# Kernel tuning notes

Measured on AMD Instinct MI355X. Metric: run time of the kernel, lower is better.

## Reference

```python
import jax, jax.numpy as jnp
import numpy as np


def setup_inputs() -> dict:
    key = jax.random.key(0)
    k1, k2, k3 = jax.random.split(key, 3)
    B, C, H, W = 32, 2048, 14, 14
    OUT = 512
    x = jax.random.normal(k1, (B, C, H, W), dtype=jnp.float32)
    gamma = jnp.zeros((1,), dtype=jnp.float32)  # nn.Parameter(torch.zeros(1))
    # 1x1 conv 2048 -> 512 (layer=4 branch), kaiming-ish scale
    conv_w = jax.random.normal(k2, (OUT, C, 1, 1), dtype=jnp.float32) * (1.0 / np.sqrt(C))
    conv_b = jax.random.normal(k3, (OUT,), dtype=jnp.float32) * 0.01
    return {"x": x, "gamma": gamma, "conv_w": conv_w, "conv_b": conv_b}


def reference(x, gamma, conv_w, conv_b):
    B, C, H, W = x.shape
    q = x.reshape(B, C, H * W)                      # [B, C, N]
    # energy[b, c, d] = <q[b,c,:], q[b,d,:]>
    energy = jnp.einsum('bcn,bdn->bcd', q, q)       # [B, C, C]
    # max-subtract trick: softmax(max - energy) along last dim
    energy_new = jnp.max(energy, axis=-1, keepdims=True) - energy
    attention = jax.nn.softmax(energy_new, axis=-1)  # [B, C, C]
    out = jnp.einsum('bcd,bdn->bcn', attention, q).reshape(B, C, H, W)
    out = gamma * out + x
    # 1x1 conv, stride 1, no padding (layer=4 branch)
    pam_out = jax.lax.conv_general_dilated(
        out, conv_w, window_strides=(1, 1), padding='VALID',
        dimension_numbers=('NCHW', 'OIHW', 'NCHW'))
    pam_out = pam_out + conv_b[None, :, None, None]
    return pam_out
```

## Files before the change

### kernel.cpp

```cpp
#include <hip/hip_runtime.h>
#include <hip/hip_bf16.h>
#include <stdint.h>

#define B_   32
#define C_   2048
#define HW_  196
#define OUT_ 512
#define KT_  128
#define NKT  (C_ / KT_)
#define BN_  64
#define PD_  4

typedef short short8 __attribute__((ext_vector_type(8)));
typedef float floatx4 __attribute__((ext_vector_type(4)));
typedef unsigned short u16;

#define VMCNT_WAIT(n) __builtin_amdgcn_s_waitcnt(0x0F70 | (n))

__device__ __forceinline__ uint32_t pack_bf16(float a, float b) {
  union { __hip_bfloat162 h; uint32_t u; } c;
  c.h = __float22bfloat162_rn(make_float2(a, b));
  return c.u;
}

__device__ __forceinline__ void async_ld16(const u16* g, void* lds_base) {
  __builtin_amdgcn_global_load_lds(
      (const __attribute__((address_space(1))) uint32_t*)g,
      (__attribute__((address_space(3))) uint32_t*)lds_base, 16, 0, 0);
}

__global__ void attn_fallback(const float* __restrict__ x, const float* __restrict__ gamma,
                              float* __restrict__ y) {
  float g = gamma[0];
  if (g == 0.0f) return;
  __shared__ float qc[HW_];
  __shared__ float e[C_];
  __shared__ float red[256];
  int tid = threadIdx.x;
  for (int cRow = blockIdx.x; cRow < C_; cRow += gridDim.x) {
    for (int b = 0; b < B_; ++b) {
      const float* q = x + (size_t)b * C_ * HW_;
      __syncthreads();
      for (int i = tid; i < HW_; i += 256) qc[i] = q[(size_t)cRow * HW_ + i];
      __syncthreads();
      for (int d = tid; d < C_; d += 256) {
        float s = 0.f;
        const float* qd = q + (size_t)d * HW_;
        for (int n = 0; n < HW_; ++n) s += qc[n] * qd[n];
        e[d] = s;
      }
      __syncthreads();
      float mn = 3.4e38f;
      for (int d = tid; d < C_; d += 256) mn = fminf(mn, e[d]);
      red[tid] = mn; __syncthreads();
      for (int s = 128; s > 0; s >>= 1) { if (tid < s) red[tid] = fminf(red[tid], red[tid + s]); __syncthreads(); }
      float emin = red[0];
      __syncthreads();
      float ps = 0.f;
      for (int d = tid; d < C_; d += 256) { float p = __expf(emin - e[d]); e[d] = p; ps += p; }
      red[tid] = ps; __syncthreads();
      for (int s = 128; s > 0; s >>= 1) { if (tid < s) red[tid] += red[tid + s]; __syncthreads(); }
      float S = red[0];
      __syncthreads();
      float invS = 1.f / S;
      for (int n = tid; n < HW_; n += 256) {
        float acc = 0.f;
        for (int d = 0; d < C_; ++d) acc += e[d] * q[(size_t)d * HW_ + n];
        y[((size_t)b * C_ + cRow) * HW_ + n] = g * acc * invS + q[(size_t)cRow * HW_ + n];
      }
    }
  }
}

__global__ __launch_bounds__(256, 3) void xposeW_kernel(
    const float* __restrict__ x, const float* __restrict__ ysrc,
    const float* __restrict__ gamma, u16* __restrict__ xT,
    const float* __restrict__ w, u16* __restrict__ wbf) {
  int tid = threadIdx.x;
  if (blockIdx.x >= 1024) {
    int gid = (blockIdx.x - 1024) * 256 + tid;
    float4 v = ((const float4*)w)[gid];
    ((uint2*)wbf)[gid] = make_uint2(pack_bf16(v.x, v.y), pack_bf16(v.z, v.w));
    return;
  }
  __shared__ float tile[64 * 197];
  const float* src = (gamma[0] != 0.f) ? ysrc : x;
  int b  = blockIdx.x >> 5;
  int c0 = (blockIdx.x & 31) * 64;
  const float* sb = src + ((size_t)b * C_ + c0) * HW_;
  for (int r = 0; r < 13; ++r) {
    int u = r * 256 + tid;
    if (u < 3136) {
      int ci = u / 49, n4 = u - ci * 49;
      float4 v = *(const float4*)(sb + (size_t)ci * HW_ + n4 * 4);
      float* tp = &tile[ci * 197 + n4 * 4];
      tp[0] = v.x; tp[1] = v.y; tp[2] = v.z; tp[3] = v.w;
    }
  }
  __syncthreads();
  u16* xTb = xT + (size_t)b * HW_ * C_ + c0;
  for (int r = 0; r < 7; ++r) {
    int u = r * 256 + tid;
    if (u < 1568) {
      int c8 = u & 7, n = u >> 3;
      const float* tp = &tile[c8 * 8 * 197 + n];
      uint4 o;
      o.x = pack_bf16(tp[0 * 197], tp[1 * 197]);
      o.y = pack_bf16(tp[2 * 197], tp[3 * 197]);
      o.z = pack_bf16(tp[4 * 197], tp[5 * 197]);
      o.w = pack_bf16(tp[6 * 197], tp[7 * 197]);
      *(uint4*)(xTb + (size_t)n * C_ + c8 * 8) = o;
    }
  }
}

__global__ __launch_bounds__(256, 2) void conv_gemm(
    const u16* __restrict__ xT, const u16* __restrict__ wbf,
    const float* __restrict__ bias, float* __restrict__ out) {

  __shared__ __align__(16) u16 Bs2[2][BN_ * KT_];

  int bid = blockIdx.x;
  int xcd = bid & 7;
  int s   = bid >> 3;
  int ot  = s & 3;
  int gl  = s >> 2;
  int grp = xcd * 16 + gl;
  int b   = grp >> 2;
  int nh  = grp & 3;
  int n0  = (nh < 3) ? nh * 64 : (HW_ - BN_);
  int oBase = ot * 128;

  int tid  = threadIdx.x;
  int wave = tid >> 6;
  int lane = tid & 63;
  int col  = lane & 15;
  int quad = lane >> 4;

  const u16* xTb  = xT + (size_t)b * HW_ * C_;
  const u16* aPtr = wbf + (size_t)(oBase + wave * 32 + col) * C_ + quad * 8;

  floatx4 acc[2][4];
#pragma unroll
  for (int m = 0; m < 2; ++m)
#pragma unroll
    for (int nt = 0; nt < 4; ++nt) { floatx4 z = {0.f, 0.f, 0.f, 0.f}; acc[m][nt] = z; }

  const u16* bPtr[PD_];
  int ldsOff[PD_];
#pragma unroll
  for (int jj = 0; jj < PD_; ++jj) {
    int rl = 4 * wave + quad + 16 * jj;
    int kc = col ^ (4 * wave + quad);
    bPtr[jj]   = xTb + (size_t)(n0 + rl) * C_ + kc * 8;
    ldsOff[jj] = (wave + 4 * jj) * 512;
  }

  uint4 aR[8];
  int aK = 0;
  auto loadA = [&]() {
#pragma unroll
    for (int m = 0; m < 2; ++m)
#pragma unroll
      for (int ks = 0; ks < 4; ++ks)
        aR[m * 4 + ks] = *(const uint4*)(aPtr + (size_t)m * 16 * C_ + aK + ks * 32);
    aK += KT_;
  };
  auto issueB = [&](u16* dst) {
#pragma unroll
    for (int jj = 0; jj < PD_; ++jj) {
      async_ld16(bPtr[jj], dst + ldsOff[jj]);
      bPtr[jj] += KT_;
    }
  };
  auto phase = [&](const u16* buf) {
    __builtin_amdgcn_s_setprio(1);
#pragma unroll
    for (int ks = 0; ks < 4; ++ks) {
      union { uint4 u; short8 v; } a0, a1;
      a0.u = aR[ks]; a1.u = aR[4 + ks];
      int chunk = (ks * 4 + quad) ^ col;
      const u16* base = buf + col * KT_ + chunk * 8;
#pragma unroll
      for (int nt = 0; nt < 4; ++nt) {
        short8 bf = *(const short8*)(base + nt * 16 * KT_);
        acc[0][nt] = __builtin_amdgcn_mfma_f32_16x16x32_bf16(a0.v, bf, acc[0][nt], 0, 0, 0);
        acc[1][nt] = __builtin_amdgcn_mfma_f32_16x16x32_bf16(a1.v, bf, acc[1][nt], 0, 0, 0);
      }
    }
    __builtin_amdgcn_s_setprio(0);
  };

  issueB(Bs2[0]);
  loadA();
  issueB(Bs2[1]);
  u16* cur = Bs2[0]; u16* nxt = Bs2[1];
#pragma unroll
  for (int kt = 0; kt < NKT - 1; ++kt) {
    VMCNT_WAIT(PD_);
    __builtin_amdgcn_s_barrier();
    phase(cur);
    loadA();
    __builtin_amdgcn_s_barrier();
    if (kt < NKT - 2) issueB(cur);
    u16* t = cur; cur = nxt; nxt = t;
  }
  VMCNT_WAIT(0);
  __builtin_amdgcn_s_barrier();
  phase(cur);

  float* outb = out + (size_t)b * OUT_ * HW_;
#pragma unroll
  for (int m = 0; m < 2; ++m)
#pragma unroll
    for (int r = 0; r < 4; ++r) {
      int o = oBase + wave * 32 + m * 16 + quad * 4 + r;
      float bv = bias[o];
      float* orow = outb + (size_t)o * HW_ + n0;
#pragma unroll
      for (int nt = 0; nt < 4; ++nt)
        orow[nt * 16 + col] = acc[m][nt][r] + bv;
    }
}

extern "C" void kernel_launch(void* const* d_in, const int* in_sizes, int n_in,
                              void* d_out, int out_size, void* d_ws, size_t ws_size,
                              hipStream_t stream) {
  const float* x      = (const float*)d_in[0];
  const float* gamma  = (const float*)d_in[1];
  const float* conv_w = (const float*)d_in[2];
  const float* conv_b = (const float*)d_in[3];
  float* out = (float*)d_out;

  const size_t wbf_bytes = (size_t)OUT_ * C_ * sizeof(u16);
  const size_t xT_bytes  = (size_t)B_ * HW_ * C_ * sizeof(u16);
  const size_t y_bytes   = (size_t)B_ * C_ * HW_ * sizeof(float);
  u16*   wbf = (u16*)d_ws;
  u16*   xT  = (u16*)((char*)d_ws + wbf_bytes);
  float* yws = (float*)((char*)d_ws + wbf_bytes + xT_bytes);
  bool have_fallback_ws = ws_size >= wbf_bytes + xT_bytes + y_bytes;
  const float* ysrc = have_fallback_ws ? (const float*)yws : x;

  if (have_fallback_ws)
    attn_fallback<<<dim3(256), dim3(256), 0, stream>>>(x, gamma, yws);
  xposeW_kernel<<<dim3(2048), dim3(256), 0, stream>>>(
      x, ysrc, gamma, xT, conv_w, wbf);
  conv_gemm<<<dim3(512), dim3(256), 0, stream>>>(xT, wbf, conv_b, out);
}
```

Measured before the change: 135.5 us.

## Switch conv GEMM to 32x32x16 MFMA with 64x128 output tiles

The conv GEMM tile changes from 128 outputs by 64 pixels to 64 outputs by 128 pixels. Each wave now computes a 32x64 sub-tile with 32x32x16 bf16 MFMAs instead of 16x16x32 ones. Each batch image is now covered by two overlapping 128-pixel column tiles instead of four 64-pixel tiles, and B-tile async loads double per stage. The aim is fewer LDS reads per MFMA and less redundant B traffic. The cost is more overlapped pixel work (256 vs 196 columns) and a larger LDS footprint per block.

```diff
diff --git a/kernel.cpp b/kernel.cpp
--- a/kernel.cpp
+++ b/kernel.cpp
@@ -8,11 +8,11 @@
 #define OUT_ 512
 #define KT_  128
 #define NKT  (C_ / KT_)
-#define BN_  64
-#define PD_  4
+#define BN_  128
+#define PD_  8
 
 typedef short short8 __attribute__((ext_vector_type(8)));
-typedef float floatx4 __attribute__((ext_vector_type(4)));
+typedef float floatx16 __attribute__((ext_vector_type(16)));
 typedef unsigned short u16;
 
 #define VMCNT_WAIT(n) __builtin_amdgcn_s_waitcnt(0x0F70 | (n))
@@ -123,35 +123,39 @@
   int bid = blockIdx.x;
   int xcd = bid & 7;
   int s   = bid >> 3;
-  int ot  = s & 3;
-  int gl  = s >> 2;
-  int grp = xcd * 16 + gl;
-  int b   = grp >> 2;
-  int nh  = grp & 3;
-  int n0  = (nh < 3) ? nh * 64 : (HW_ - BN_);
-  int oBase = ot * 128;
+  int ot  = s & 7;
+  int g   = ((s >> 3) << 3) | xcd;
+  int b   = g >> 1;
+  int nh  = g & 1;
+  int n0  = nh * (HW_ - BN_);
+  int oBase = ot * 64;
 
   int tid  = threadIdx.x;
   int wave = tid >> 6;
   int lane = tid & 63;
-  int col  = lane & 15;
   int quad = lane >> 4;
+  int hi   = lane >> 5;
+  int l15  = lane & 15;
+  int l31  = lane & 31;
+  int osub = wave & 1;
+  int nsub = wave >> 1;
 
   const u16* xTb  = xT + (size_t)b * HW_ * C_;
-  const u16* aPtr = wbf + (size_t)(oBase + wave * 32 + col) * C_ + quad * 8;
-
-  floatx4 acc[2][4];
-#pragma unroll
-  for (int m = 0; m < 2; ++m)
-#pragma unroll
-    for (int nt = 0; nt < 4; ++nt) { floatx4 z = {0.f, 0.f, 0.f, 0.f}; acc[m][nt] = z; }
+  const u16* aPtr = wbf + (size_t)(oBase + osub * 32 + l31) * C_ + hi * 8;
+
+  floatx16 acc[2];
+#pragma unroll
+  for (int ntl = 0; ntl < 2; ++ntl) {
+    floatx16 z = {0.f,0.f,0.f,0.f,0.f,0.f,0.f,0.f,0.f,0.f,0.f,0.f,0.f,0.f,0.f,0.f};
+    acc[ntl] = z;
+  }
 
   const u16* bPtr[PD_];
   int ldsOff[PD_];
 #pragma unroll
   for (int jj = 0; jj < PD_; ++jj) {
     int rl = 4 * wave + quad + 16 * jj;
-    int kc = col ^ (4 * wave + quad);
+    int kc = l15 ^ (4 * wave + quad);
     bPtr[jj]   = xTb + (size_t)(n0 + rl) * C_ + kc * 8;
     ldsOff[jj] = (wave + 4 * jj) * 512;
   }
@@ -160,10 +164,8 @@
   int aK = 0;
   auto loadA = [&]() {
 #pragma unroll
-    for (int m = 0; m < 2; ++m)
-#pragma unroll
-      for (int ks = 0; ks < 4; ++ks)
-        aR[m * 4 + ks] = *(const uint4*)(aPtr + (size_t)m * 16 * C_ + aK + ks * 32);
+    for (int ks = 0; ks < 8; ++ks)
+      aR[ks] = *(const uint4*)(aPtr + aK + ks * 16);
     aK += KT_;
   };
   auto issueB = [&](u16* dst) {
@@ -173,19 +175,17 @@
       bPtr[jj] += KT_;
     }
   };
+  const int rowU16 = (nsub * 64 + l31) * KT_;
   auto phase = [&](const u16* buf) {
     __builtin_amdgcn_s_setprio(1);
 #pragma unroll
-    for (int ks = 0; ks < 4; ++ks) {
-      union { uint4 u; short8 v; } a0, a1;
-      a0.u = aR[ks]; a1.u = aR[4 + ks];
-      int chunk = (ks * 4 + quad) ^ col;
-      const u16* base = buf + col * KT_ + chunk * 8;
-#pragma unroll
-      for (int nt = 0; nt < 4; ++nt) {
-        short8 bf = *(const short8*)(base + nt * 16 * KT_);
-        acc[0][nt] = __builtin_amdgcn_mfma_f32_16x16x32_bf16(a0.v, bf, acc[0][nt], 0, 0, 0);
-        acc[1][nt] = __builtin_amdgcn_mfma_f32_16x16x32_bf16(a1.v, bf, acc[1][nt], 0, 0, 0);
+    for (int ks = 0; ks < 8; ++ks) {
+      union { uint4 u; short8 v; } af; af.u = aR[ks];
+      int chunk = (2 * ks + hi) ^ l15;
+#pragma unroll
+      for (int ntl = 0; ntl < 2; ++ntl) {
+        short8 bf = *(const short8*)(buf + rowU16 + ntl * 32 * KT_ + chunk * 8);
+        acc[ntl] = __builtin_amdgcn_mfma_f32_32x32x16_bf16(af.v, bf, acc[ntl], 0, 0, 0);
       }
     }
     __builtin_amdgcn_s_setprio(0);
@@ -211,16 +211,13 @@
 
   float* outb = out + (size_t)b * OUT_ * HW_;
 #pragma unroll
-  for (int m = 0; m < 2; ++m)
-#pragma unroll
-    for (int r = 0; r < 4; ++r) {
-      int o = oBase + wave * 32 + m * 16 + quad * 4 + r;
-      float bv = bias[o];
-      float* orow = outb + (size_t)o * HW_ + n0;
-#pragma unroll
-      for (int nt = 0; nt < 4; ++nt)
-        orow[nt * 16 + col] = acc[m][nt][r] + bv;
-    }
+  for (int reg = 0; reg < 16; ++reg) {
+    int o = oBase + osub * 32 + (reg & 3) + 8 * (reg >> 2) + 4 * hi;
+    float bv = bias[o];
+    float* orow = outb + (size_t)o * HW_ + n0 + nsub * 64 + l31;
+    orow[0]  = acc[0][reg] + bv;
+    orow[32] = acc[1][reg] + bv;
+  }
 }
 
 extern "C" void kernel_launch(void* const* d_in, const int* in_sizes, int n_in,
```

New measurement: 144.6 us. 6.7% more time.
